# Kernel optimization log

Measured on AMD Instinct MI355X. Metric: run time of the kernel, lower is better.

Reference implementation:

```python
import jax, jax.numpy as jnp
import numpy as np

NUM_CLASSES = 24


def setup_inputs() -> dict:
    key = jax.random.key(0)
    k1, k2 = jax.random.split(key)
    data = jax.random.normal(k1, (8, 128, 128, 128), dtype=jnp.float32)
    label = jax.random.randint(k2, (8, 512, 512), 0, NUM_CLASSES, dtype=jnp.int64)
    return {"data": data, "label": label}


def reference(data, label):
    B, C, h, w = data.shape
    _, H, W = label.shape
    # nearest-neighbor interpolate to (H, W): torch 'nearest' uses floor(dst * src/dst)
    ri = (jnp.arange(H) * h) // H
    ci = (jnp.arange(W) * w) // W
    data_up = data[:, :, ri[:, None], ci[None, :]]  # [B, C, H, W]
    valid = label != -1                              # ignore mask
    lab = jnp.where(valid, label, 0)
    # scatter-add instead of one-hot + einsum (same math)
    seg = (lab + jnp.arange(B, dtype=lab.dtype)[:, None, None] * NUM_CLASSES).reshape(-1)
    x = (data_up * valid[:, None, :, :].astype(data.dtype))  # zero out ignored pixels
    x = x.transpose(0, 2, 3, 1).reshape(B * H * W, C)        # [B*H*W, C]
    sums = jax.ops.segment_sum(x, seg, num_segments=B * NUM_CLASSES)
    sums = sums.reshape(B, NUM_CLASSES, C)                   # [B, N, C]
    counts = jax.ops.segment_sum(valid.reshape(-1).astype(jnp.float32), seg,
                                 num_segments=B * NUM_CLASSES)
    counts = counts.reshape(B, NUM_CLASSES)                  # [B, N]
    feature = (sums / (counts[:, :, None] + 1e-8)).transpose(0, 2, 1)  # [B, C, N]
    mask = (counts > 0).astype(jnp.float32)                  # [B, N]
    return feature, mask
```

## Files before the change

kernel.cpp:

```cpp
#include <hip/hip_runtime.h>

#define NCLS 24
#define NB 8
#define NCH 128
#define WLO 128
#define WHI 512
#define CELLS (128*128)
#define SUBS 2
#define BLOCKS_PER_B (256 / SUBS)
#define NBLK (NB * BLOCKS_PER_B)
#define KCH (NCLS * NCH)
#define NF (NB * KCH)
#define WPITCH 72

typedef _Float16 f16x4 __attribute__((ext_vector_type(4)));
typedef _Float16 f16x8 __attribute__((ext_vector_type(8)));
typedef float    f32x4 __attribute__((ext_vector_type(4)));

__global__ __launch_bounds__(256, 4)
void fm_main(const float* __restrict__ data, const int* __restrict__ label,
             float* __restrict__ part, float* __restrict__ cpart)
{
    __shared__ unsigned histu[NCLS * 64];
    __shared__ _Float16 w16[32 * WPITCH];
    __shared__ _Float16 tile[NCH * 64];

    const int bid  = blockIdx.x;
    const int b    = bid / BLOCKS_PER_B;
    const int grp  = bid % BLOCKS_PER_B;
    const int tid  = threadIdx.x;

    const int q    = tid & 15;
    const int chb  = tid >> 4;
    const int r    = tid >> 6;
    const int cl   = tid & 63;
    const int w    = tid >> 6;
    const int lane = tid & 63;

    const float* dbase = data  + (size_t)b * NCH * CELLS;
    const int*   lbase = label + (size_t)b * (WHI * WHI);

    f32x4 acc[2][2];
#pragma unroll
    for (int mt = 0; mt < 2; ++mt)
#pragma unroll
        for (int nt = 0; nt < 2; ++nt) acc[mt][nt] = (f32x4){0.f, 0.f, 0.f, 0.f};

    float4 v[8];
    int4 lv;

    {
        const int sub = grp * SUBS;
        const int y = sub >> 1, x0 = (sub & 1) << 6;
        const int cb = y * WLO + x0;
#pragma unroll
        for (int k = 0; k < 8; ++k)
            v[k] = *reinterpret_cast<const float4*>(dbase + (size_t)(chb + k * 16) * CELLS + cb + q * 4);
        lv = *reinterpret_cast<const int4*>(lbase + (size_t)(4 * y + r) * WHI + x0 * 4 + cl * 4);
    }

    unsigned cacc = 0;

#pragma unroll
    for (int s = 0; s < SUBS; ++s) {
#pragma unroll
        for (int k = 0; k < 6; ++k) histu[tid + k * 256] = 0u;
        __syncthreads();

        if ((unsigned)lv.x < 24u) atomicAdd(&histu[lv.x * 64 + cl], 1u);
        if ((unsigned)lv.y < 24u) atomicAdd(&histu[lv.y * 64 + cl], 1u);
        if ((unsigned)lv.z < 24u) atomicAdd(&histu[lv.z * 64 + cl], 1u);
        if ((unsigned)lv.w < 24u) atomicAdd(&histu[lv.w * 64 + cl], 1u);

#pragma unroll
        for (int k = 0; k < 8; ++k) {
            const int ch = chb + k * 16;
            f16x4 hv;
            hv[0] = (_Float16)v[k].x; hv[1] = (_Float16)v[k].y;
            hv[2] = (_Float16)v[k].z; hv[3] = (_Float16)v[k].w;
            const int idx = ch * 64 + ((((q >> 1) ^ (ch & 7)) << 3) | ((q & 1) << 2));
            *reinterpret_cast<f16x4*>(&tile[idx]) = hv;
        }
        __syncthreads();

        if (s + 1 < SUBS) {
            const int sub = grp * SUBS + s + 1;
            const int y = sub >> 1, x0 = (sub & 1) << 6;
            const int cb = y * WLO + x0;
#pragma unroll
            for (int k = 0; k < 8; ++k)
                v[k] = *reinterpret_cast<const float4*>(dbase + (size_t)(chb + k * 16) * CELLS + cb + q * 4);
            lv = *reinterpret_cast<const int4*>(lbase + (size_t)(4 * y + r) * WHI + x0 * 4 + cl * 4);
        }

#pragma unroll
        for (int k = 0; k < 6; ++k) {
            const int e = tid + k * 256;
            const int cls = e >> 6, c = e & 63;
            w16[cls * WPITCH + c] = (_Float16)(float)histu[e];
        }
        if (tid < 96) {
            const int cls = tid >> 2, qq = tid & 3;
#pragma unroll
            for (int i = 0; i < 16; ++i)
                cacc += histu[cls * 64 + qq * 16 + ((i + cls) & 15)];
        }
        __syncthreads();

        f16x8 af[2][2], bf[2][2];
#pragma unroll
        for (int mt = 0; mt < 2; ++mt)
#pragma unroll
            for (int kt = 0; kt < 2; ++kt)
                af[mt][kt] = *reinterpret_cast<const f16x8*>(
                    &w16[(mt * 16 + (lane & 15)) * WPITCH + kt * 32 + (lane >> 4) * 8]);
#pragma unroll
        for (int nt = 0; nt < 2; ++nt)
#pragma unroll
            for (int kt = 0; kt < 2; ++kt) {
                const int row = w * 32 + nt * 16 + (lane & 15);
                const int g   = kt * 4 + (lane >> 4);
                bf[nt][kt] = *reinterpret_cast<const f16x8*>(
                    &tile[row * 64 + ((g ^ (row & 7)) << 3)]);
            }
#pragma unroll
        for (int mt = 0; mt < 2; ++mt)
#pragma unroll
            for (int nt = 0; nt < 2; ++nt)
#pragma unroll
                for (int kt = 0; kt < 2; ++kt)
                    acc[mt][nt] = __builtin_amdgcn_mfma_f32_16x16x32_f16(
                        af[mt][kt], bf[nt][kt], acc[mt][nt], 0, 0, 0);
        __syncthreads();
    }

    float* pblk = part + (size_t)bid * KCH;
#pragma unroll
    for (int mt = 0; mt < 2; ++mt)
#pragma unroll
        for (int nt = 0; nt < 2; ++nt)
#pragma unroll
            for (int rg = 0; rg < 4; ++rg) {
                const int cls = mt * 16 + (lane >> 4) * 4 + rg;
                const int ch  = w * 32 + nt * 16 + (lane & 15);
                if (cls < NCLS) pblk[cls * NCH + ch] = acc[mt][nt][rg];
            }
    if (tid < 96) cpart[(size_t)bid * 96 + tid] = (float)cacc;
}

__global__ __launch_bounds__(256)
void fm_final(const float* __restrict__ part, const float* __restrict__ cpart,
              float* __restrict__ out)
{
    __shared__ float cred[128];
    const int b   = blockIdx.x / NCLS;
    const int cls = blockIdx.x % NCLS;
    const int t   = threadIdx.x;

    float s = 0.f;
    if (t < 128) {
        const float* pb = part + (size_t)(b * BLOCKS_PER_B) * KCH + cls * NCH + t;
#pragma unroll 4
        for (int g = 0; g < BLOCKS_PER_B; ++g) s += pb[(size_t)g * KCH];
    } else {
        const int g = t - 128;
        const float* cb = cpart + (size_t)(b * BLOCKS_PER_B + g) * 96 + cls * 4;
        cred[g] = cb[0] + cb[1] + cb[2] + cb[3];
    }
    __syncthreads();
#pragma unroll
    for (int st = 64; st >= 1; st >>= 1) {
        if (t >= 128 && (t - 128) < st) cred[t - 128] += cred[t - 128 + st];
        __syncthreads();
    }
    const float cnt = cred[0];
    if (t < 128) out[(size_t)b * KCH + t * NCLS + cls] = s / (cnt + 1e-8f);
    if (t == 128) out[NF + b * NCLS + cls] = (cnt > 0.f) ? 1.f : 0.f;
}

extern "C" void kernel_launch(void* const* d_in, const int* in_sizes, int n_in,
                              void* d_out, int out_size, void* d_ws, size_t ws_size,
                              hipStream_t stream) {
    const float* data  = (const float*)d_in[0];
    const int*   label = (const int*)d_in[1];
    float* out   = (float*)d_out;
    float* part  = (float*)d_ws;
    float* cpart = part + (size_t)NBLK * KCH;

    fm_main<<<dim3(NBLK), dim3(256), 0, stream>>>(data, label, part, cpart);
    fm_final<<<dim3(NB * NCLS), dim3(256), 0, stream>>>(part, cpart, out);
}
```

Measured before the change: 32.27 us.

## Use one sub-tile per block with fp16 partials and swizzled histogram

Each main-kernel block now handles a single 64-cell sub-tile instead of two, which doubles the block count and raises the occupancy hint. The MFMA A-operand is built directly from a swizzled uint histogram, dropping the separate fp16 weight buffer and one barrier. Per-block partial sums are stored as fp16 and the count partials are reduced per class. Twice as many partial rows means the final kernel reads more of them, though fp16 halves their size. Storing partial sums in fp16 risks precision loss.

```diff
diff --git a/kernel.cpp b/kernel.cpp
--- a/kernel.cpp
+++ b/kernel.cpp
@@ -6,28 +6,27 @@
 #define WLO 128
 #define WHI 512
 #define CELLS (128*128)
-#define SUBS 2
-#define BLOCKS_PER_B (256 / SUBS)
-#define NBLK (NB * BLOCKS_PER_B)
+#define SUBT 256
+#define NBLK (NB * SUBT)
 #define KCH (NCLS * NCH)
 #define NF (NB * KCH)
-#define WPITCH 72
 
 typedef _Float16 f16x4 __attribute__((ext_vector_type(4)));
 typedef _Float16 f16x8 __attribute__((ext_vector_type(8)));
 typedef float    f32x4 __attribute__((ext_vector_type(4)));
 
-__global__ __launch_bounds__(256, 4)
+#define HIDX(c_, e_) (((c_) << 6) + ((e_) ^ (((c_) & 15) << 2)))
+
+__global__ __launch_bounds__(256, 6)
 void fm_main(const float* __restrict__ data, const int* __restrict__ label,
-             float* __restrict__ part, float* __restrict__ cpart)
+             _Float16* __restrict__ part, float* __restrict__ cpart)
 {
-    __shared__ unsigned histu[NCLS * 64];
-    __shared__ _Float16 w16[32 * WPITCH];
+    __shared__ unsigned histu[32 * 64];
     __shared__ _Float16 tile[NCH * 64];
 
     const int bid  = blockIdx.x;
-    const int b    = bid / BLOCKS_PER_B;
-    const int grp  = bid % BLOCKS_PER_B;
+    const int b    = bid >> 8;
+    const int grp  = bid & 255;
     const int tid  = threadIdx.x;
 
     const int q    = tid & 15;
@@ -37,104 +36,85 @@
     const int w    = tid >> 6;
     const int lane = tid & 63;
 
+    const int y  = grp >> 1;
+    const int x0 = (grp & 1) << 6;
+    const int cb = y * WLO + x0;
+
     const float* dbase = data  + (size_t)b * NCH * CELLS;
     const int*   lbase = label + (size_t)b * (WHI * WHI);
+
+    float4 v[8];
+#pragma unroll
+    for (int k = 0; k < 8; ++k)
+        v[k] = *reinterpret_cast<const float4*>(dbase + (size_t)(chb + k * 16) * CELLS + cb + q * 4);
+    const int4 lv = *reinterpret_cast<const int4*>(lbase + (size_t)(4 * y + r) * WHI + x0 * 4 + cl * 4);
+
+#pragma unroll
+    for (int k = 0; k < 8; ++k) histu[tid + k * 256] = 0u;
+    __syncthreads();
+
+    if ((unsigned)lv.x < 24u) atomicAdd(&histu[HIDX(lv.x, cl)], 1u);
+    if ((unsigned)lv.y < 24u) atomicAdd(&histu[HIDX(lv.y, cl)], 1u);
+    if ((unsigned)lv.z < 24u) atomicAdd(&histu[HIDX(lv.z, cl)], 1u);
+    if ((unsigned)lv.w < 24u) atomicAdd(&histu[HIDX(lv.w, cl)], 1u);
+
+#pragma unroll
+    for (int k = 0; k < 8; ++k) {
+        const int ch = chb + k * 16;
+        f16x4 hv;
+        hv[0] = (_Float16)v[k].x; hv[1] = (_Float16)v[k].y;
+        hv[2] = (_Float16)v[k].z; hv[3] = (_Float16)v[k].w;
+        const int idx = ch * 64 + ((((q >> 1) ^ (ch & 7)) << 3) | ((q & 1) << 2));
+        *reinterpret_cast<f16x4*>(&tile[idx]) = hv;
+    }
+    __syncthreads();
+
+    unsigned ucnt = 0;
+    if (tid < NCLS) {
+#pragma unroll
+        for (int i = 0; i < 64; ++i) ucnt += histu[(tid << 6) + ((i + tid * 3) & 63)];
+    }
+
+    f16x8 af[2][2];
+#pragma unroll
+    for (int mt = 0; mt < 2; ++mt)
+#pragma unroll
+        for (int kt = 0; kt < 2; ++kt) {
+            const int cls = mt * 16 + (lane & 15);
+            const int e0  = kt * 32 + (lane >> 4) * 8;
+            const uint4 u0 = *reinterpret_cast<const uint4*>(&histu[HIDX(cls, e0)]);
+            const uint4 u1 = *reinterpret_cast<const uint4*>(&histu[HIDX(cls, e0 + 4)]);
+            f16x8 a;
+            a[0] = (_Float16)(float)u0.x; a[1] = (_Float16)(float)u0.y;
+            a[2] = (_Float16)(float)u0.z; a[3] = (_Float16)(float)u0.w;
+            a[4] = (_Float16)(float)u1.x; a[5] = (_Float16)(float)u1.y;
+            a[6] = (_Float16)(float)u1.z; a[7] = (_Float16)(float)u1.w;
+            af[mt][kt] = a;
+        }
+
+    f16x8 bf[2][2];
+#pragma unroll
+    for (int nt = 0; nt < 2; ++nt)
+#pragma unroll
+        for (int kt = 0; kt < 2; ++kt) {
+            const int row = w * 32 + nt * 16 + (lane & 15);
+            const int g   = kt * 4 + (lane >> 4);
+            bf[nt][kt] = *reinterpret_cast<const f16x8*>(&tile[row * 64 + ((g ^ (row & 7)) << 3)]);
+        }
 
     f32x4 acc[2][2];
 #pragma unroll
     for (int mt = 0; mt < 2; ++mt)
 #pragma unroll
-        for (int nt = 0; nt < 2; ++nt) acc[mt][nt] = (f32x4){0.f, 0.f, 0.f, 0.f};
-
-    float4 v[8];
-    int4 lv;
-
-    {
-        const int sub = grp * SUBS;
-        const int y = sub >> 1, x0 = (sub & 1) << 6;
-        const int cb = y * WLO + x0;
+        for (int nt = 0; nt < 2; ++nt) {
+            acc[mt][nt] = (f32x4){0.f, 0.f, 0.f, 0.f};
 #pragma unroll
-        for (int k = 0; k < 8; ++k)
-            v[k] = *reinterpret_cast<const float4*>(dbase + (size_t)(chb + k * 16) * CELLS + cb + q * 4);
-        lv = *reinterpret_cast<const int4*>(lbase + (size_t)(4 * y + r) * WHI + x0 * 4 + cl * 4);
-    }
-
-    unsigned cacc = 0;
-
-#pragma unroll
-    for (int s = 0; s < SUBS; ++s) {
-#pragma unroll
-        for (int k = 0; k < 6; ++k) histu[tid + k * 256] = 0u;
-        __syncthreads();
-
-        if ((unsigned)lv.x < 24u) atomicAdd(&histu[lv.x * 64 + cl], 1u);
-        if ((unsigned)lv.y < 24u) atomicAdd(&histu[lv.y * 64 + cl], 1u);
-        if ((unsigned)lv.z < 24u) atomicAdd(&histu[lv.z * 64 + cl], 1u);
-        if ((unsigned)lv.w < 24u) atomicAdd(&histu[lv.w * 64 + cl], 1u);
-
-#pragma unroll
-        for (int k = 0; k < 8; ++k) {
-            const int ch = chb + k * 16;
-            f16x4 hv;
-            hv[0] = (_Float16)v[k].x; hv[1] = (_Float16)v[k].y;
-            hv[2] = (_Float16)v[k].z; hv[3] = (_Float16)v[k].w;
-            const int idx = ch * 64 + ((((q >> 1) ^ (ch & 7)) << 3) | ((q & 1) << 2));
-            *reinterpret_cast<f16x4*>(&tile[idx]) = hv;
-        }
-        __syncthreads();
-
-        if (s + 1 < SUBS) {
-            const int sub = grp * SUBS + s + 1;
-            const int y = sub >> 1, x0 = (sub & 1) << 6;
-            const int cb = y * WLO + x0;
-#pragma unroll
-            for (int k = 0; k < 8; ++k)
-                v[k] = *reinterpret_cast<const float4*>(dbase + (size_t)(chb + k * 16) * CELLS + cb + q * 4);
-            lv = *reinterpret_cast<const int4*>(lbase + (size_t)(4 * y + r) * WHI + x0 * 4 + cl * 4);
+            for (int kt = 0; kt < 2; ++kt)
+                acc[mt][nt] = __builtin_amdgcn_mfma_f32_16x16x32_f16(
+                    af[mt][kt], bf[nt][kt], acc[mt][nt], 0, 0, 0);
         }
 
-#pragma unroll
-        for (int k = 0; k < 6; ++k) {
-            const int e = tid + k * 256;
-            const int cls = e >> 6, c = e & 63;
-            w16[cls * WPITCH + c] = (_Float16)(float)histu[e];
-        }
-        if (tid < 96) {
-            const int cls = tid >> 2, qq = tid & 3;
-#pragma unroll
-            for (int i = 0; i < 16; ++i)
-                cacc += histu[cls * 64 + qq * 16 + ((i + cls) & 15)];
-        }
-        __syncthreads();
-
-        f16x8 af[2][2], bf[2][2];
-#pragma unroll
-        for (int mt = 0; mt < 2; ++mt)
-#pragma unroll
-            for (int kt = 0; kt < 2; ++kt)
-                af[mt][kt] = *reinterpret_cast<const f16x8*>(
-                    &w16[(mt * 16 + (lane & 15)) * WPITCH + kt * 32 + (lane >> 4) * 8]);
-#pragma unroll
-        for (int nt = 0; nt < 2; ++nt)
-#pragma unroll
-            for (int kt = 0; kt < 2; ++kt) {
-                const int row = w * 32 + nt * 16 + (lane & 15);
-                const int g   = kt * 4 + (lane >> 4);
-                bf[nt][kt] = *reinterpret_cast<const f16x8*>(
-                    &tile[row * 64 + ((g ^ (row & 7)) << 3)]);
-            }
-#pragma unroll
-        for (int mt = 0; mt < 2; ++mt)
-#pragma unroll
-            for (int nt = 0; nt < 2; ++nt)
-#pragma unroll
-                for (int kt = 0; kt < 2; ++kt)
-                    acc[mt][nt] = __builtin_amdgcn_mfma_f32_16x16x32_f16(
-                        af[mt][kt], bf[nt][kt], acc[mt][nt], 0, 0, 0);
-        __syncthreads();
-    }
-
-    float* pblk = part + (size_t)bid * KCH;
+    _Float16* pblk = part + (size_t)bid * KCH;
 #pragma unroll
     for (int mt = 0; mt < 2; ++mt)
 #pragma unroll
@@ -143,13 +123,13 @@
             for (int rg = 0; rg < 4; ++rg) {
                 const int cls = mt * 16 + (lane >> 4) * 4 + rg;
                 const int ch  = w * 32 + nt * 16 + (lane & 15);
-                if (cls < NCLS) pblk[cls * NCH + ch] = acc[mt][nt][rg];
+                if (cls < NCLS) pblk[cls * NCH + ch] = (_Float16)acc[mt][nt][rg];
             }
-    if (tid < 96) cpart[(size_t)bid * 96 + tid] = (float)cacc;
+    if (tid < NCLS) cpart[(size_t)bid * NCLS + tid] = (float)ucnt;
 }
 
 __global__ __launch_bounds__(256)
-void fm_final(const float* __restrict__ part, const float* __restrict__ cpart,
+void fm_final(const _Float16* __restrict__ part, const float* __restrict__ cpart,
               float* __restrict__ out)
 {
     __shared__ float cred[128];
@@ -159,13 +139,13 @@
 
     float s = 0.f;
     if (t < 128) {
-        const float* pb = part + (size_t)(b * BLOCKS_PER_B) * KCH + cls * NCH + t;
-#pragma unroll 4
-        for (int g = 0; g < BLOCKS_PER_B; ++g) s += pb[(size_t)g * KCH];
+        const _Float16* pb = part + (size_t)(b * SUBT) * KCH + cls * NCH + t;
+#pragma unroll 8
+        for (int g = 0; g < SUBT; ++g) s += (float)pb[(size_t)g * KCH];
     } else {
-        const int g = t - 128;
-        const float* cb = cpart + (size_t)(b * BLOCKS_PER_B + g) * 96 + cls * 4;
-        cred[g] = cb[0] + cb[1] + cb[2] + cb[3];
+        const int g2 = (t - 128) * 2;
+        const float* cbp = cpart + (size_t)(b * SUBT) * NCLS + cls;
+        cred[t - 128] = cbp[(size_t)g2 * NCLS] + cbp[(size_t)(g2 + 1) * NCLS];
     }
     __syncthreads();
 #pragma unroll
@@ -183,9 +163,9 @@
                               hipStream_t stream) {
     const float* data  = (const float*)d_in[0];
     const int*   label = (const int*)d_in[1];
-    float* out   = (float*)d_out;
-    float* part  = (float*)d_ws;
-    float* cpart = part + (size_t)NBLK * KCH;
+    float*     out   = (float*)d_out;
+    _Float16*  part  = (_Float16*)d_ws;
+    float*     cpart = (float*)(part + (size_t)NBLK * KCH);
 
     fm_main<<<dim3(NBLK), dim3(256), 0, stream>>>(data, label, part, cpart);
     fm_final<<<dim3(NB * NCLS), dim3(256), 0, stream>>>(part, cpart, out);
```

After: 34.63 us. 1.07x slower.
